# Performance work log

Hardware: AMD Instinct MI355X
Metric: run time of the kernel (lower is better)

Reference implementation:

```python
import jax, jax.numpy as jnp
import numpy as np

B, LQ, LK, D = 16, 2048, 2048, 256
NEG = -1e10


def setup_inputs() -> dict:
    key = jax.random.key(0)
    k1, k2, k3, k4, k5 = jax.random.split(key, 5)
    scale = 1.0 / np.sqrt(D)
    return {
        "x": jax.random.normal(k1, (B, LQ, D), dtype=jnp.float32),
        "y": jax.random.normal(k2, (B, LK, D), dtype=jnp.float32),
        "mask": jnp.zeros((B, LK), dtype=bool),  # True = padded key position
        "Wq": jax.random.normal(k3, (D, D), dtype=jnp.float32) * scale,
        "Wk": jax.random.normal(k4, (D, D), dtype=jnp.float32) * scale,
        "Wv": jax.random.normal(k5, (D, D), dtype=jnp.float32) * scale,
    }


def reference(x, y, mask, Wq, Wk, Wv):
    # nn.Linear: out = in @ W.T (no bias)
    q = jnp.einsum('bqd,ed->bqe', x, Wq)   # [B, LQ, D]
    k = jnp.einsum('bkd,ed->bke', y, Wk)   # [B, LK, D]
    v = jnp.einsum('bkd,ed->bke', y, Wv)   # [B, LK, D]
    # cdist (p=2) via GEMM expansion: ||q||^2 + ||k||^2 - 2 q.k
    qn = jnp.sum(q * q, axis=-1)                              # [B, LQ]
    kn = jnp.sum(k * k, axis=-1)                              # [B, LK]
    d2 = qn[:, :, None] + kn[:, None, :] - 2.0 * jnp.einsum('bqd,bkd->bqk', q, k)
    dist = jnp.sqrt(jnp.maximum(d2, 0.0))                     # [B, LQ, LK]
    scores = jnp.exp(-dist)
    # masked_fill: where original mask is True, set pre-softmax score to -1e10
    scores = jnp.where(mask[:, None, :], NEG, scores)
    attn = jax.nn.softmax(scores, axis=-1)                    # [B, LQ, LK]
    att_out = jnp.einsum('bqk,bkd->bqd', attn, v)             # [B, LQ, D]
    return (att_out, attn)
```

## Files before the change

### kernel.cpp

```cpp
#include <hip/hip_runtime.h>
#include <stdint.h>

#define B_   16
#define L_   2048
#define D_   256
#define NROW (B_*L_)

#define EPAD 40
#define TPAD 66

typedef __attribute__((ext_vector_type(8)))  short s8v;
typedef __attribute__((ext_vector_type(4)))  float f4v;
typedef __attribute__((ext_vector_type(16))) float f16v;

__device__ __forceinline__ unsigned short f2b(float f) {
    unsigned u = __builtin_bit_cast(unsigned, f);
    return (unsigned short)((u + 0x7fffu + ((u >> 16) & 1u)) >> 16);
}

__device__ __forceinline__ void gl16(const void* g, void* l) {
    __builtin_amdgcn_global_load_lds(
        (const __attribute__((address_space(1))) unsigned int*)g,
        (__attribute__((address_space(3))) unsigned int*)l, 16, 0, 0);
}

__global__ __launch_bounds__(256) void qkv_kernel(
    const float* __restrict__ x, const float* __restrict__ y,
    const float* __restrict__ Wq, const float* __restrict__ Wk, const float* __restrict__ Wv,
    unsigned short* __restrict__ Qb, unsigned short* __restrict__ Kb,
    unsigned short* __restrict__ Vt,
    float* __restrict__ qn, float* __restrict__ kn)
{
    __shared__ unsigned short Xs[64*256];
    __shared__ unsigned short Ws[64*256];
    __shared__ unsigned short Ts[64*TPAD];

    const int t    = threadIdx.x;
    const int r0   = blockIdx.x * 64;
    const int type = blockIdx.y;

    const float* X = (type == 0) ? x : y;
    const float* W = (type == 0) ? Wq : (type == 1) ? Wk : Wv;

    #pragma unroll
    for (int p = 0; p < 16; ++p) {
        int idx  = p*256 + t;
        int row  = idx >> 6;
        int half = idx & 1;
        int blk  = (idx & 63) >> 1;
        int c4   = blk*8 + half*4;
        float4 vx = *(const float4*)(X + (size_t)(r0+row)*D_ + c4);
        uint2 px;
        px.x = (unsigned)f2b(vx.x) | ((unsigned)f2b(vx.y) << 16);
        px.y = (unsigned)f2b(vx.z) | ((unsigned)f2b(vx.w) << 16);
        *(uint2*)(Xs + row*256 + (blk ^ (row & 15))*8 + half*4) = px;
    }

    const int w = t >> 6, lane = t & 63, q16 = lane & 15, quad = lane >> 4;
    const int m0 = w * 16;

    float p4[4] = {0.f, 0.f, 0.f, 0.f};
    const f4v z4 = {0.f, 0.f, 0.f, 0.f};

    for (int ct = 0; ct < 4; ++ct) {
        const int e0 = ct * 64;
        __syncthreads();
        #pragma unroll
        for (int p = 0; p < 16; ++p) {
            int idx  = p*256 + t;
            int row  = idx >> 6;
            int half = idx & 1;
            int blk  = (idx & 63) >> 1;
            int c4   = blk*8 + half*4;
            float4 vw = *(const float4*)(W + (size_t)(e0+row)*D_ + c4);
            uint2 pw;
            pw.x = (unsigned)f2b(vw.x) | ((unsigned)f2b(vw.y) << 16);
            pw.y = (unsigned)f2b(vw.z) | ((unsigned)f2b(vw.w) << 16);
            *(uint2*)(Ws + row*256 + (blk ^ (row & 15))*8 + half*4) = pw;
        }
        __syncthreads();

        f4v acc[4];
        #pragma unroll
        for (int n = 0; n < 4; ++n) acc[n] = z4;
        #pragma unroll
        for (int c = 0; c < 8; ++c) {
            s8v a = *(const s8v*)(Xs + (m0 + q16)*256 + (((c*4+quad) ^ q16)*8));
            #pragma unroll
            for (int n = 0; n < 4; ++n) {
                s8v bb = *(const s8v*)(Ws + (n*16 + q16)*256 + (((c*4+quad) ^ q16)*8));
                acc[n] = __builtin_amdgcn_mfma_f32_16x16x32_bf16(a, bb, acc[n], 0, 0, 0);
            }
        }

        if (type < 2) {
            unsigned short* Out = (type == 0) ? Qb : Kb;
            #pragma unroll
            for (int n = 0; n < 4; ++n)
                #pragma unroll
                for (int r = 0; r < 4; ++r) {
                    float v = acc[n][r];
                    p4[r] += v * v;
                    Out[(size_t)(r0 + m0 + quad*4 + r)*D_ + e0 + n*16 + q16] = f2b(v);
                }
        } else {
            #pragma unroll
            for (int n = 0; n < 4; ++n)
                #pragma unroll
                for (int r = 0; r < 4; ++r)
                    Ts[(m0 + quad*4 + r)*TPAD + n*16 + q16] = f2b(acc[n][r]);
            __syncthreads();
            int j    = t >> 2;
            int kseg = t & 3;
            unsigned pk[8];
            #pragma unroll
            for (int i = 0; i < 8; ++i) {
                unsigned lo = Ts[(kseg*16 + 2*i    )*TPAD + j];
                unsigned hi = Ts[(kseg*16 + 2*i + 1)*TPAD + j];
                pk[i] = lo | (hi << 16);
            }
            int bb_ = r0 >> 11;
            int k0g = r0 & (L_ - 1);
            unsigned short* dst = Vt + (size_t)(bb_*D_ + e0 + j)*L_ + k0g + kseg*16;
            *(uint4*)dst       = make_uint4(pk[0], pk[1], pk[2], pk[3]);
            *((uint4*)dst + 1) = make_uint4(pk[4], pk[5], pk[6], pk[7]);
        }
    }

    if (type < 2) {
        float* norm = (type == 0) ? qn : kn;
        #pragma unroll
        for (int r = 0; r < 4; ++r) {
            float v = p4[r];
            v += __shfl_xor(v, 1, 16);
            v += __shfl_xor(v, 2, 16);
            v += __shfl_xor(v, 4, 16);
            v += __shfl_xor(v, 8, 16);
            if (q16 == 0) norm[r0 + m0 + quad*4 + r] = v;
        }
    }
}

__device__ __forceinline__ void stage_K(const unsigned short* Kb, unsigned short* ks,
                                        int bk, int k0, int w, int lane) {
    #pragma unroll
    for (int p = 0; p < 8; ++p) {
        int slot = p*128 + w*64 + lane;
        int row  = slot >> 5;
        int blk  = slot & 31;
        gl16(Kb + (size_t)(bk + k0 + row)*D_ + ((blk ^ (row & 15))*8),
             ks + (size_t)(p*128 + w*64)*8);
    }
}
__device__ __forceinline__ void stage_V(const unsigned short* Vt, unsigned short* vs,
                                        int bD, int k0, int w, int lane) {
    #pragma unroll
    for (int p = 0; p < 8; ++p) {
        int slot = p*128 + w*64 + lane;
        int d    = slot >> 2;
        int blk  = slot & 3;
        gl16(Vt + (size_t)(bD + d)*L_ + k0 + ((blk ^ ((d >> 1) & 3))*8),
             vs + (size_t)(p*128 + w*64)*8);
    }
}

__global__ __launch_bounds__(128) void attnpv_kernel(
    const unsigned short* __restrict__ Qb, const unsigned short* __restrict__ Kb,
    const unsigned short* __restrict__ Vt,
    const float* __restrict__ qn, const float* __restrict__ kn,
    const unsigned char* __restrict__ mask,
    unsigned short* __restrict__ Eb,
    float* __restrict__ rowsum, float* __restrict__ att_out)
{
    __shared__ unsigned short Ks[2][32*256];
    __shared__ unsigned short Vs[2][256*32];
    __shared__ unsigned short Es[2][32*EPAD];

    const int t  = threadIdx.x;
    const int q0 = blockIdx.x * 64;
    const int b  = blockIdx.y;
    const int bk = b * L_;
    const int bD = b * D_;
    const int w    = t >> 6;
    const int lane = t & 63;
    const int col  = lane & 31;
    const int h    = lane >> 5;

    const int qrow = bk + q0 + w*32;

    s8v qa[16];
    #pragma unroll
    for (int c = 0; c < 16; ++c)
        qa[c] = *(const s8v*)(Qb + (size_t)(qrow + col)*D_ + c*16 + h*8);

    float qnr[16];
    #pragma unroll
    for (int reg = 0; reg < 16; ++reg)
        qnr[reg] = qn[qrow + (reg & 3) + 8*(reg >> 2) + 4*h];

    unsigned short* ebase = Eb + (size_t)(qrow + (lane >> 1))*L_ + (lane & 1)*16;
    const unsigned short* esrc = &Es[w][(lane >> 1)*EPAD + (lane & 1)*16];

    float rs[16];
    #pragma unroll
    for (int reg = 0; reg < 16; ++reg) rs[reg] = 0.f;
    f16v O[8];
    #pragma unroll
    for (int n = 0; n < 8; ++n)
        #pragma unroll
        for (int reg = 0; reg < 16; ++reg) O[n][reg] = 0.f;

    stage_K(Kb, Ks[0], bk, 0, w, lane);
    stage_V(Vt, Vs[0], bD, 0, w, lane);
    for (int kt = 0; kt < 64; ++kt) {
        const int k0 = kt * 32;
        const int cur = kt & 1;
        __syncthreads();
        if (kt < 63) {
            stage_K(Kb, Ks[cur ^ 1], bk, k0 + 32, w, lane);
            stage_V(Vt, Vs[cur ^ 1], bD, k0 + 32, w, lane);
        }

        const float kc = kn[bk + k0 + col];
        const int   mk = mask[bk + k0 + col];

        f16v s;
        #pragma unroll
        for (int reg = 0; reg < 16; ++reg) s[reg] = 0.f;
        #pragma unroll
        for (int c = 0; c < 16; ++c) {
            s8v bb = *(const s8v*)(Ks[cur] + col*256 + (((2*c + h) ^ (col & 15))*8));
            s = __builtin_amdgcn_mfma_f32_32x32x16_bf16(qa[c], bb, s, 0, 0, 0);
        }

        #pragma unroll
        for (int reg = 0; reg < 16; ++reg) {
            float d2 = qnr[reg] + kc - 2.0f * s[reg];
            float dist = __builtin_amdgcn_sqrtf(fmaxf(d2, 0.f));
            float E = mk ? 0.f : __expf(__expf(-dist));
            rs[reg] += E;
            Es[w][((reg & 3) + 8*(reg >> 2) + 4*h)*EPAD + col] = f2b(E);
        }

        s8v af0 = *(const s8v*)(&Es[w][col*EPAD + h*8]);
        s8v af1 = *(const s8v*)(&Es[w][col*EPAD + 16 + h*8]);
        #pragma unroll
        for (int n = 0; n < 8; ++n) {
            int d  = n*32 + col;
            int sw = (d >> 1) & 3;
            s8v vb0 = *(const s8v*)(Vs[cur] + d*32 + ((h ^ sw)*8));
            s8v vb1 = *(const s8v*)(Vs[cur] + d*32 + (((2 + h) ^ sw)*8));
            O[n] = __builtin_amdgcn_mfma_f32_32x32x16_bf16(af0, vb0, O[n], 0, 0, 0);
            O[n] = __builtin_amdgcn_mfma_f32_32x32x16_bf16(af1, vb1, O[n], 0, 0, 0);
        }

        *(s8v*)(ebase + k0)     = *(const s8v*)esrc;
        *(s8v*)(ebase + k0 + 8) = *(const s8v*)(esrc + 8);
    }

    float inv[16];
    #pragma unroll
    for (int reg = 0; reg < 16; ++reg) {
        float v = rs[reg];
        v += __shfl_xor(v, 1, 32);
        v += __shfl_xor(v, 2, 32);
        v += __shfl_xor(v, 4, 32);
        v += __shfl_xor(v, 8, 32);
        v += __shfl_xor(v, 16, 32);
        if (col == 0) rowsum[qrow + (reg & 3) + 8*(reg >> 2) + 4*h] = v;
        inv[reg] = 1.0f / v;
    }

    #pragma unroll
    for (int n = 0; n < 8; ++n)
        #pragma unroll
        for (int reg = 0; reg < 16; ++reg)
            att_out[(size_t)(qrow + (reg & 3) + 8*(reg >> 2) + 4*h)*D_ + n*32 + col]
                = O[n][reg] * inv[reg];
}

__global__ __launch_bounds__(256) void norm_kernel(
    const unsigned short* __restrict__ Eb,
    const float* __restrict__ rowsum,
    float* __restrict__ attn_out)
{
    const int row = blockIdx.x;
    const int t   = threadIdx.x;
    const float inv = 1.0f / rowsum[row];
    const size_t base = (size_t)row * L_ + t*8;

    s8v e = *(const s8v*)(Eb + base);
    float4 o0, o1;
    o0.x = __builtin_bit_cast(float, ((unsigned)(unsigned short)e[0]) << 16) * inv;
    o0.y = __builtin_bit_cast(float, ((unsigned)(unsigned short)e[1]) << 16) * inv;
    o0.z = __builtin_bit_cast(float, ((unsigned)(unsigned short)e[2]) << 16) * inv;
    o0.w = __builtin_bit_cast(float, ((unsigned)(unsigned short)e[3]) << 16) * inv;
    o1.x = __builtin_bit_cast(float, ((unsigned)(unsigned short)e[4]) << 16) * inv;
    o1.y = __builtin_bit_cast(float, ((unsigned)(unsigned short)e[5]) << 16) * inv;
    o1.z = __builtin_bit_cast(float, ((unsigned)(unsigned short)e[6]) << 16) * inv;
    o1.w = __builtin_bit_cast(float, ((unsigned)(unsigned short)e[7]) << 16) * inv;
    *(float4*)(attn_out + base)     = o0;
    *(float4*)(attn_out + base + 4) = o1;
}

extern "C" void kernel_launch(void* const* d_in, const int* in_sizes, int n_in,
                              void* d_out, int out_size, void* d_ws, size_t ws_size,
                              hipStream_t stream) {
    (void)in_sizes; (void)n_in; (void)out_size; (void)ws_size;
    const float* x  = (const float*)d_in[0];
    const float* y  = (const float*)d_in[1];
    const unsigned char* mask = (const unsigned char*)d_in[2];
    const float* Wq = (const float*)d_in[3];
    const float* Wk = (const float*)d_in[4];
    const float* Wv = (const float*)d_in[5];

    char* ws = (char*)d_ws;
    unsigned short* Qb = (unsigned short*)ws;
    unsigned short* Kb = Qb + (size_t)NROW * D_;
    unsigned short* Vt = Kb + (size_t)NROW * D_;
    float* qn     = (float*)(ws + 3 * (size_t)NROW * D_ * 2);
    float* kn     = qn + NROW;
    float* rowsum = kn + NROW;
    unsigned short* Eb = (unsigned short*)(rowsum + NROW);

    float* att_out = (float*)d_out;
    float* attn    = att_out + (size_t)NROW * D_;

    qkv_kernel<<<dim3(512, 3), 256, 0, stream>>>(x, y, Wq, Wk, Wv,
                                                 Qb, Kb, Vt, qn, kn);
    attnpv_kernel<<<dim3(32, 16), 128, 0, stream>>>(Qb, Kb, Vt, qn, kn, mask,
                                                    Eb, rowsum, att_out);
    norm_kernel<<<dim3(NROW), 256, 0, stream>>>(Eb, rowsum, attn);
}
```

Baseline: 597.0 us.

## Load K and V fragments directly from global memory, drop LDS staging

The attention kernel no longer double-buffers K and V tiles in shared memory through global_load_lds. Each single-wave block now reads its MFMA B-operands for K and V straight from global memory into registers, so barriers disappear and the launch grid doubles to 64x16 blocks of 64 threads. The float-to-bf16 conversion of E changes from round-to-nearest to plain truncation. In exchange, K and V are no longer shared between waves, so global and L2 traffic per block rises, the V loads are strided, register pressure goes up, and the truncation adds a small precision change.

```diff
diff --git a/kernel.cpp b/kernel.cpp
--- a/kernel.cpp
+++ b/kernel.cpp
@@ -16,12 +16,6 @@
 __device__ __forceinline__ unsigned short f2b(float f) {
     unsigned u = __builtin_bit_cast(unsigned, f);
     return (unsigned short)((u + 0x7fffu + ((u >> 16) & 1u)) >> 16);
-}
-
-__device__ __forceinline__ void gl16(const void* g, void* l) {
-    __builtin_amdgcn_global_load_lds(
-        (const __attribute__((address_space(1))) unsigned int*)g,
-        (__attribute__((address_space(3))) unsigned int*)l, 16, 0, 0);
 }
 
 __global__ __launch_bounds__(256) void qkv_kernel(
@@ -141,30 +135,7 @@
     }
 }
 
-__device__ __forceinline__ void stage_K(const unsigned short* Kb, unsigned short* ks,
-                                        int bk, int k0, int w, int lane) {
-    #pragma unroll
-    for (int p = 0; p < 8; ++p) {
-        int slot = p*128 + w*64 + lane;
-        int row  = slot >> 5;
-        int blk  = slot & 31;
-        gl16(Kb + (size_t)(bk + k0 + row)*D_ + ((blk ^ (row & 15))*8),
-             ks + (size_t)(p*128 + w*64)*8);
-    }
-}
-__device__ __forceinline__ void stage_V(const unsigned short* Vt, unsigned short* vs,
-                                        int bD, int k0, int w, int lane) {
-    #pragma unroll
-    for (int p = 0; p < 8; ++p) {
-        int slot = p*128 + w*64 + lane;
-        int d    = slot >> 2;
-        int blk  = slot & 3;
-        gl16(Vt + (size_t)(bD + d)*L_ + k0 + ((blk ^ ((d >> 1) & 3))*8),
-             vs + (size_t)(p*128 + w*64)*8);
-    }
-}
-
-__global__ __launch_bounds__(128) void attnpv_kernel(
+__global__ __launch_bounds__(64) void attnpv_kernel(
     const unsigned short* __restrict__ Qb, const unsigned short* __restrict__ Kb,
     const unsigned short* __restrict__ Vt,
     const float* __restrict__ qn, const float* __restrict__ kn,
@@ -172,21 +143,17 @@
     unsigned short* __restrict__ Eb,
     float* __restrict__ rowsum, float* __restrict__ att_out)
 {
-    __shared__ unsigned short Ks[2][32*256];
-    __shared__ unsigned short Vs[2][256*32];
-    __shared__ unsigned short Es[2][32*EPAD];
-
-    const int t  = threadIdx.x;
-    const int q0 = blockIdx.x * 64;
-    const int b  = blockIdx.y;
-    const int bk = b * L_;
-    const int bD = b * D_;
-    const int w    = t >> 6;
-    const int lane = t & 63;
+    __shared__ unsigned short Es[32*EPAD];
+
+    const int lane = threadIdx.x;
+    const int q0   = blockIdx.x * 32;
+    const int b    = blockIdx.y;
+    const int bk   = b * L_;
+    const int bD   = b * D_;
     const int col  = lane & 31;
     const int h    = lane >> 5;
 
-    const int qrow = bk + q0 + w*32;
+    const int qrow = bk + q0;
 
     s8v qa[16];
     #pragma unroll
@@ -199,7 +166,7 @@
         qnr[reg] = qn[qrow + (reg & 3) + 8*(reg >> 2) + 4*h];
 
     unsigned short* ebase = Eb + (size_t)(qrow + (lane >> 1))*L_ + (lane & 1)*16;
-    const unsigned short* esrc = &Es[w][(lane >> 1)*EPAD + (lane & 1)*16];
+    const unsigned short* esrc = &Es[(lane >> 1)*EPAD + (lane & 1)*16];
 
     float rs[16];
     #pragma unroll
@@ -210,26 +177,27 @@
         #pragma unroll
         for (int reg = 0; reg < 16; ++reg) O[n][reg] = 0.f;
 
-    stage_K(Kb, Ks[0], bk, 0, w, lane);
-    stage_V(Vt, Vs[0], bD, 0, w, lane);
     for (int kt = 0; kt < 64; ++kt) {
         const int k0 = kt * 32;
-        const int cur = kt & 1;
-        __syncthreads();
-        if (kt < 63) {
-            stage_K(Kb, Ks[cur ^ 1], bk, k0 + 32, w, lane);
-            stage_V(Vt, Vs[cur ^ 1], bD, k0 + 32, w, lane);
+
+        s8v vf[16];
+        #pragma unroll
+        for (int n = 0; n < 8; ++n) {
+            const unsigned short* vr = Vt + (size_t)(bD + n*32 + col)*L_ + k0 + h*8;
+            vf[2*n]     = *(const s8v*)vr;
+            vf[2*n + 1] = *(const s8v*)(vr + 16);
         }
 
         const float kc = kn[bk + k0 + col];
         const int   mk = mask[bk + k0 + col];
 
+        const unsigned short* kr = Kb + (size_t)(bk + k0 + col)*D_ + h*8;
         f16v s;
         #pragma unroll
         for (int reg = 0; reg < 16; ++reg) s[reg] = 0.f;
         #pragma unroll
         for (int c = 0; c < 16; ++c) {
-            s8v bb = *(const s8v*)(Ks[cur] + col*256 + (((2*c + h) ^ (col & 15))*8));
+            s8v bb = *(const s8v*)(kr + c*16);
             s = __builtin_amdgcn_mfma_f32_32x32x16_bf16(qa[c], bb, s, 0, 0, 0);
         }
 
@@ -239,19 +207,16 @@
             float dist = __builtin_amdgcn_sqrtf(fmaxf(d2, 0.f));
             float E = mk ? 0.f : __expf(__expf(-dist));
             rs[reg] += E;
-            Es[w][((reg & 3) + 8*(reg >> 2) + 4*h)*EPAD + col] = f2b(E);
-        }
-
-        s8v af0 = *(const s8v*)(&Es[w][col*EPAD + h*8]);
-        s8v af1 = *(const s8v*)(&Es[w][col*EPAD + 16 + h*8]);
+            Es[((reg & 3) + 8*(reg >> 2) + 4*h)*EPAD + col] =
+                (unsigned short)(__builtin_bit_cast(unsigned, E) >> 16);
+        }
+
+        s8v af0 = *(const s8v*)(&Es[col*EPAD + h*8]);
+        s8v af1 = *(const s8v*)(&Es[col*EPAD + 16 + h*8]);
         #pragma unroll
         for (int n = 0; n < 8; ++n) {
-            int d  = n*32 + col;
-            int sw = (d >> 1) & 3;
-            s8v vb0 = *(const s8v*)(Vs[cur] + d*32 + ((h ^ sw)*8));
-            s8v vb1 = *(const s8v*)(Vs[cur] + d*32 + (((2 + h) ^ sw)*8));
-            O[n] = __builtin_amdgcn_mfma_f32_32x32x16_bf16(af0, vb0, O[n], 0, 0, 0);
-            O[n] = __builtin_amdgcn_mfma_f32_32x32x16_bf16(af1, vb1, O[n], 0, 0, 0);
+            O[n] = __builtin_amdgcn_mfma_f32_32x32x16_bf16(af0, vf[2*n],     O[n], 0, 0, 0);
+            O[n] = __builtin_amdgcn_mfma_f32_32x32x16_bf16(af1, vf[2*n + 1], O[n], 0, 0, 0);
         }
 
         *(s8v*)(ebase + k0)     = *(const s8v*)esrc;
@@ -328,7 +293,7 @@
 
     qkv_kernel<<<dim3(512, 3), 256, 0, stream>>>(x, y, Wq, Wk, Wv,
                                                  Qb, Kb, Vt, qn, kn);
-    attnpv_kernel<<<dim3(32, 16), 128, 0, stream>>>(Qb, Kb, Vt, qn, kn, mask,
-                                                    Eb, rowsum, att_out);
+    attnpv_kernel<<<dim3(64, 16), 64, 0, stream>>>(Qb, Kb, Vt, qn, kn, mask,
+                                                   Eb, rowsum, att_out);
     norm_kernel<<<dim3(NROW), 256, 0, stream>>>(Eb, rowsum, attn);
 }
```

Result: slower. 713.8 us (+19.6%).
